# Kernel tuning notes

Measured on AMD Instinct MI355X. Metric: run time of the kernel, lower is better.

## Reference

```python
import jax, jax.numpy as jnp
import numpy as np

SIGMA_E, SIGMA_I, K_E, K_I = 0.6, 1.2, 0.8, 1.0
PM_STEPS, DT, BETA = 4, 0.15, 1.0
EPS = 1e-4


def setup_inputs() -> dict:
    key = jax.random.key(0)
    ks = jax.random.split(key, 12)
    B, d_in, d_lat, ch, d_out, n_c = 4096, 784, 8, 32, 10, 16
    inp = {
        "x": jax.random.normal(ks[0], (B, d_in), dtype=jnp.float32),
        "W1": jax.random.normal(ks[1], (d_in, 128), dtype=jnp.float32) * 0.03,
        "b1": jnp.zeros((128,), jnp.float32),
        "W2": jax.random.normal(ks[2], (128, d_lat), dtype=jnp.float32) * 0.08,
        "b2": jnp.zeros((d_lat,), jnp.float32),
        "centers": jax.random.normal(ks[3], (n_c, d_lat), dtype=jnp.float32) * 0.7,
        "mus": jnp.ones((n_c,), jnp.float32) * 0.5,
        "Wp": jax.random.normal(ks[4], (d_lat, ch), dtype=jnp.float32) * 0.3,
        "bp": jnp.zeros((ch,), jnp.float32),
        "Wr": jax.random.normal(ks[5], (ch, d_out), dtype=jnp.float32) * 0.15,
        "br": jnp.zeros((d_out,), jnp.float32),
        "T": 5,
    }
    return inp


def grad_ln_n(z, centers, mus):
    # z: [B,d], centers: [C,d], mus: [C]
    rvec = z[:, None, :] - centers[None, :, :]          # [B,C,d]
    r = jnp.sqrt(jnp.sum(rvec * rvec, axis=-1) + EPS)   # [B,C]
    n = 1.0 + jnp.sum(mus[None, :] / r, axis=1)          # [B]
    g = -jnp.sum((mus[None, :] / (r ** 3))[:, :, None] * rvec, axis=1)  # [B,d]
    return g / n[:, None]


def pm_field(z, centers, mus):
    for _ in range(PM_STEPS):
        z = jnp.clip(z + DT * BETA * grad_ln_n(z, centers, mus), -3.0, 3.0)
    return z


def lateral_kernel(z):
    # squared pairwise distances via the norm trick (avoids [B,B,d])
    sq = jnp.sum(z * z, axis=1)
    dist2 = jnp.maximum(sq[:, None] + sq[None, :] - 2.0 * (z @ z.T), 0.0)
    K = K_E * jnp.exp(-dist2 / (2.0 * SIGMA_E ** 2)) - K_I * jnp.exp(-dist2 / (2.0 * SIGMA_I ** 2))
    return jax.lax.stop_gradient(K)  # torch.no_grad in original


def reference(x, W1, b1, W2, b2, centers, mus, Wp, bp, Wr, br, T):
    B = x.shape[0]
    z = jnp.tanh(x.reshape(B, -1) @ W1 + b1) @ W2 + b2   # encoder
    h = jnp.zeros((B, Wr.shape[0]), x.dtype)
    for _ in range(T):
        z = pm_field(z, centers, mus)
        h = 0.9 * h + 0.1 * jnp.tanh(z @ Wp + bp)
        h = h + 0.05 * (lateral_kernel(z) @ h)
        y = h @ Wr + br
    return y
```

## Files before the change

### kernel.cpp

```cpp
#include <hip/hip_runtime.h>
#include <math.h>

#define NB    4096
#define DIN   784
#define DH    128
#define DL    8
#define NC    16
#define NCH   32
#define DO    10
#define TSTEPS 5

#define KH_ROWS   128
#define KH_JSLICE 64
#define KH_P      (NB / KH_JSLICE)
#define ENC_G     7

typedef float v2f __attribute__((ext_vector_type(2)));


__global__ __launch_bounds__(256) void enc1_kernel(const float* __restrict__ x,
    const float* __restrict__ W1, double* __restrict__ P)
{
    __shared__ float xsT[56][36];
    __shared__ float wss[56][128];
    const int tid = threadIdx.x;
    const int m0 = blockIdx.x * 32;
    const int kbeg = blockIdx.y * 112;
    const int cg = tid & 31, rg = tid >> 5;
    const int c0 = cg << 2, r0 = rg << 2;
    double acc[4][4] = {};
    for (int it = 0; it < 2; ++it) {
        const int k0 = kbeg + it * 56;
        __syncthreads();
        for (int l = tid; l < 448; l += 256) {
            int row = l / 14, f = l % 14;
            float4 v = *(const float4*)(x + (m0 + row) * DIN + k0 + f * 4);
            int kk = f * 4;
            xsT[kk][row] = v.x; xsT[kk + 1][row] = v.y;
            xsT[kk + 2][row] = v.z; xsT[kk + 3][row] = v.w;
        }
        for (int l = tid; l < 56 * 32; l += 256) {
            int kk = l >> 5, c = (l & 31) << 2;
            *(float4*)&wss[kk][c] = *(const float4*)(W1 + (k0 + kk) * DH + c);
        }
        __syncthreads();
#pragma unroll 8
        for (int kk = 0; kk < 56; ++kk) {
            const float4 xv = *(const float4*)&xsT[kk][r0];
            const float4 wv = *(const float4*)&wss[kk][c0];
            const double xr[4] = {(double)xv.x, (double)xv.y, (double)xv.z, (double)xv.w};
            const double wr[4] = {(double)wv.x, (double)wv.y, (double)wv.z, (double)wv.w};
#pragma unroll
            for (int i = 0; i < 4; ++i)
#pragma unroll
                for (int j = 0; j < 4; ++j)
                    acc[i][j] += xr[i] * wr[j];
        }
    }
    double* Pr = P + (size_t)blockIdx.y * (NB * DH);
#pragma unroll
    for (int i = 0; i < 4; ++i) {
        double* dst = Pr + (m0 + r0 + i) * DH + c0;
        *(double2*)dst       = make_double2(acc[i][0], acc[i][1]);
        *(double2*)(dst + 2) = make_double2(acc[i][2], acc[i][3]);
    }
}

__global__ __launch_bounds__(256) void enc2_kernel(const double* __restrict__ P,
    const float* __restrict__ b1, const float* __restrict__ W2,
    const float* __restrict__ b2, double* __restrict__ zbuf)
{
    __shared__ double As[16][132];
    __shared__ double W2d[DH * DL];
    const int tid = threadIdx.x;
    const int m0 = blockIdx.x * 16;
    for (int l = tid; l < DH * DL; l += 256) W2d[l] = (double)W2[l];
    for (int l = tid; l < 16 * 128; l += 256) {
        int row = l >> 7, k = l & 127;
        double v = (double)b1[k];
#pragma unroll
        for (int s = 0; s < ENC_G; ++s)
            v += P[(size_t)s * NB * DH + (m0 + row) * DH + k];
        As[row][k] = tanh(v);
    }
    __syncthreads();
    const int row = tid >> 4, d = (tid >> 1) & 7, half = tid & 1;
    double a = 0.0;
#pragma unroll 8
    for (int i = 0; i < 64; ++i) {
        const int k = half + (i << 1);
        a += As[row][k] * W2d[k * 8 + d];
    }
    a += __shfl_xor(a, 1);
    if (half == 0) zbuf[(m0 + row) * DL + d] = a + (double)b2[d];
}

__global__ __launch_bounds__(256) void enc_fused_kernel(const float* __restrict__ x,
    const float* __restrict__ W1, const float* __restrict__ b1,
    const float* __restrict__ W2, const float* __restrict__ b2,
    double* __restrict__ zbuf)
{
    __shared__ float  xsT[56][9];
    __shared__ float  wss[56][128];
    __shared__ double Asd[8][131];
    __shared__ double W2d[DH * DL];
    const int tid = threadIdx.x;
    const int m0 = blockIdx.x * 8;
    const int cg = tid & 31, rg = tid >> 5;
    const int c0 = cg << 2;
    for (int l = tid; l < DH * DL; l += 256) W2d[l] = (double)W2[l];
    double acc[4] = {};
    for (int it = 0; it < 14; ++it) {
        const int k0 = it * 56;
        __syncthreads();
        if (tid < 112) {
            int row = tid / 14, f = tid % 14;
            float4 v = *(const float4*)(x + (m0 + row) * DIN + k0 + f * 4);
            int kk = f * 4;
            xsT[kk][row] = v.x; xsT[kk + 1][row] = v.y;
            xsT[kk + 2][row] = v.z; xsT[kk + 3][row] = v.w;
        }
        for (int l = tid; l < 56 * 32; l += 256) {
            int kk = l >> 5, c = (l & 31) << 2;
            *(float4*)&wss[kk][c] = *(const float4*)(W1 + (k0 + kk) * DH + c);
        }
        __syncthreads();
#pragma unroll 8
        for (int kk = 0; kk < 56; ++kk) {
            const double xv = (double)xsT[kk][rg];
            const float4 wv = *(const float4*)&wss[kk][c0];
            acc[0] += xv * (double)wv.x;
            acc[1] += xv * (double)wv.y;
            acc[2] += xv * (double)wv.z;
            acc[3] += xv * (double)wv.w;
        }
    }
    __syncthreads();
#pragma unroll
    for (int j = 0; j < 4; ++j)
        Asd[rg][c0 + j] = tanh(acc[j] + (double)b1[c0 + j]);
    __syncthreads();
    {
        const int row = tid >> 5, d = (tid >> 2) & 7, kq = tid & 3;
        double a = 0.0;
#pragma unroll 8
        for (int i = 0; i < 32; ++i) {
            const int k = kq + (i << 2);
            a += Asd[row][k] * W2d[k * 8 + d];
        }
        a += __shfl_xor(a, 1);
        a += __shfl_xor(a, 2);
        if (kq == 0) zbuf[(m0 + row) * DL + d] = a + (double)b2[d];
    }
}

__global__ __launch_bounds__(64) void pmh_kernel(double* __restrict__ zbuf,
    const float* __restrict__ centers, const float* __restrict__ mus,
    const float* __restrict__ Wp, const float* __restrict__ bp,
    double* __restrict__ hB, float* __restrict__ zf, float* __restrict__ sqf,
    float* __restrict__ hAf, const float* __restrict__ part, int first)
{
    const int tid = threadIdx.x;
    const int lane = tid & 15;
    const int s = tid >> 4;
    const int i = blockIdx.x * 4 + s;
    double cz[8];
#pragma unroll
    for (int d = 0; d < 8; ++d) cz[d] = (double)centers[lane * DL + d];
    const double mu = (double)mus[lane];
    double z[8];
#pragma unroll
    for (int p = 0; p < 4; ++p) {
        double2 v = *(const double2*)(zbuf + i * DL + p * 2);
        z[p * 2] = v.x; z[p * 2 + 1] = v.y;
    }
#pragma unroll
    for (int st = 0; st < 4; ++st) {
        double rv[8];
        double ss = 1e-4;
#pragma unroll
        for (int d = 0; d < 8; ++d) { rv[d] = z[d] - cz[d]; ss += rv[d] * rv[d]; }
        double rinv = rsqrt(ss);
        double mr = mu * rinv;
        double n = mr;
        double mr3 = mr * (rinv * rinv);
        double g[8];
#pragma unroll
        for (int d = 0; d < 8; ++d) g[d] = -mr3 * rv[d];
#pragma unroll
        for (int m = 1; m < 16; m <<= 1) {
            n += __shfl_xor(n, m);
#pragma unroll
            for (int d = 0; d < 8; ++d) g[d] += __shfl_xor(g[d], m);
        }
        double sc = 0.15 / (1.0 + n);
#pragma unroll
        for (int d = 0; d < 8; ++d) z[d] = fmin(3.0, fmax(-3.0, z[d] + sc * g[d]));
    }
    if (lane == 0) {
        double sq = 0.0;
#pragma unroll
        for (int d = 0; d < 8; ++d) sq += z[d] * z[d];
        sqf[i] = (float)sq;
#pragma unroll
        for (int p = 0; p < 4; ++p)
            *(double2*)(zbuf + i * DL + p * 2) = make_double2(z[p * 2], z[p * 2 + 1]);
        float4 a = make_float4((float)z[0], (float)z[1], (float)z[2], (float)z[3]);
        float4 b = make_float4((float)z[4], (float)z[5], (float)z[6], (float)z[7]);
        *(float4*)(zf + i * DL)     = a;
        *(float4*)(zf + i * DL + 4) = b;
    }
#pragma unroll
    for (int cc = 0; cc < 2; ++cc) {
        const int c = lane + cc * 16;
        double a = (double)bp[c];
#pragma unroll
        for (int d = 0; d < 8; ++d) a += z[d] * (double)Wp[d * NCH + c];
        double ph = (double)tanhf((float)a);
        double prev = 0.0;
        if (!first) {
            prev = hB[i * NCH + c];
            if (part) {
                double sp = 0.0;
#pragma unroll 8
                for (int p = 0; p < KH_P; ++p)
                    sp += (double)part[(size_t)p * (NB * NCH) + i * NCH + c];
                prev += 0.05 * sp;
            }
        }
        double hv = 0.9 * prev + 0.1 * ph;
        hAf[i * NCH + c] = (float)hv;
        hB[i * NCH + c] = hv;
    }
}

#define SM_Z   0
#define SM_SQ  512
#define SM_H   576
#define SM_ALL 4224
__global__ __launch_bounds__(256) void kh_kernel(const float* __restrict__ zf,
    const float* __restrict__ sqf, const float* __restrict__ hAf,
    double* __restrict__ hB, float* __restrict__ part)
{
    __shared__ float smem[SM_ALL];
    const int tid = threadIdx.x;
    const int wave = tid >> 6, lane = tid & 63;
    const int row0 = blockIdx.x * KH_ROWS + lane;
    const int j0 = blockIdx.y * KH_JSLICE;
    float zr0[8], zr1[8];
    {
        float4 a = *(const float4*)(zf + row0 * 8);
        float4 b = *(const float4*)(zf + row0 * 8 + 4);
        zr0[0] = a.x; zr0[1] = a.y; zr0[2] = a.z; zr0[3] = a.w;
        zr0[4] = b.x; zr0[5] = b.y; zr0[6] = b.z; zr0[7] = b.w;
        float4 c = *(const float4*)(zf + (row0 + 64) * 8);
        float4 d = *(const float4*)(zf + (row0 + 64) * 8 + 4);
        zr1[0] = c.x; zr1[1] = c.y; zr1[2] = c.z; zr1[3] = c.w;
        zr1[4] = d.x; zr1[5] = d.y; zr1[6] = d.z; zr1[7] = d.w;
    }
    const float sq0 = sqf[row0], sq1 = sqf[row0 + 64];
    const float invI = 1.0f / 2.88f;
    if (tid < 128) {
        int jj = tid >> 1, p = (tid & 1) << 2;
        *(float4*)&smem[SM_Z + jj * 8 + p] = *(const float4*)(zf + (j0 + jj) * 8 + p);
    }
    if (tid < KH_JSLICE) smem[SM_SQ + tid] = sqf[j0 + tid];
    for (int l = tid; l < KH_JSLICE * 8; l += 256) {
        int jh = l >> 3, p = (l & 7) << 2;
        *(float4*)&smem[SM_H + jh * 32 + p] = *(const float4*)(hAf + (j0 + jh) * NCH + p);
    }
    __syncthreads();
    v2f a0[16], a1[16];
#pragma unroll
    for (int k = 0; k < 16; ++k) { a0[k] = (v2f)(0.f); a1[k] = (v2f)(0.f); }
    const int jjbeg = wave * 16;
#pragma unroll 2
    for (int q = 0; q < 16; ++q) {
        const int jj = jjbeg + q;
        const float4 a = *(const float4*)&smem[SM_Z + jj * 8];
        const float4 b = *(const float4*)&smem[SM_Z + jj * 8 + 4];
        const float sqj = smem[SM_SQ + jj];
        float dot0 = zr0[0] * a.x + zr0[1] * a.y + zr0[2] * a.z + zr0[3] * a.w
                   + zr0[4] * b.x + zr0[5] * b.y + zr0[6] * b.z + zr0[7] * b.w;
        float dot1 = zr1[0] * a.x + zr1[1] * a.y + zr1[2] * a.z + zr1[3] * a.w
                   + zr1[4] * b.x + zr1[5] * b.y + zr1[6] * b.z + zr1[7] * b.w;
        float d20 = fmaxf(sq0 + sqj - 2.0f * dot0, 0.0f);
        float d21 = fmaxf(sq1 + sqj - 2.0f * dot1, 0.0f);
        float e0 = __expf(-d20 * invI), e1 = __expf(-d21 * invI);
        float t0 = e0 * e0, t1 = e1 * e1;
        float K0 = 0.8f * (t0 * t0) - e0;
        float K1 = 0.8f * (t1 * t1) - e1;
        const v2f K0v = {K0, K0}, K1v = {K1, K1};
        const v2f* hrow = (const v2f*)&smem[SM_H + jj * 32];
#pragma unroll
        for (int k = 0; k < 16; k += 2) {
            const v2f h0 = hrow[k], h1 = hrow[k + 1];
            a0[k]     += K0v * h0; a0[k + 1] += K0v * h1;
            a1[k]     += K1v * h0; a1[k + 1] += K1v * h1;
        }
    }
    float* acc0 = (float*)a0;
    float* acc1 = (float*)a1;
    __syncthreads();
    if (wave == 1) {
#pragma unroll
        for (int c = 0; c < 32; ++c) { smem[lane * 33 + c] = acc0[c]; smem[(lane + 64) * 33 + c] = acc1[c]; }
    }
    __syncthreads();
    if (wave == 0) {
#pragma unroll
        for (int c = 0; c < 32; ++c) { acc0[c] += smem[lane * 33 + c]; acc1[c] += smem[(lane + 64) * 33 + c]; }
    }
    __syncthreads();
    if (wave == 3) {
#pragma unroll
        for (int c = 0; c < 32; ++c) { smem[lane * 33 + c] = acc0[c]; smem[(lane + 64) * 33 + c] = acc1[c]; }
    }
    __syncthreads();
    if (wave == 2) {
#pragma unroll
        for (int c = 0; c < 32; ++c) { acc0[c] += smem[lane * 33 + c]; acc1[c] += smem[(lane + 64) * 33 + c]; }
    }
    __syncthreads();
    if (wave == 2) {
#pragma unroll
        for (int c = 0; c < 32; ++c) { smem[lane * 33 + c] = acc0[c]; smem[(lane + 64) * 33 + c] = acc1[c]; }
    }
    __syncthreads();
    if (wave == 0) {
#pragma unroll
        for (int c = 0; c < 32; ++c) { acc0[c] += smem[lane * 33 + c]; acc1[c] += smem[(lane + 64) * 33 + c]; }
        if (part) {
            float* p0 = part + (size_t)blockIdx.y * (NB * NCH) + row0 * NCH;
            float* p1 = p0 + 64 * NCH;
#pragma unroll
            for (int c = 0; c < 32; c += 4) {
                *(float4*)(p0 + c) = make_float4(acc0[c], acc0[c + 1], acc0[c + 2], acc0[c + 3]);
                *(float4*)(p1 + c) = make_float4(acc1[c], acc1[c + 1], acc1[c + 2], acc1[c + 3]);
            }
        } else {
#pragma unroll
            for (int c = 0; c < 32; ++c) {
                atomicAdd(&hB[row0 * NCH + c], 0.05 * (double)acc0[c]);
                atomicAdd(&hB[(row0 + 64) * NCH + c], 0.05 * (double)acc1[c]);
            }
        }
    }
}

__global__ __launch_bounds__(256) void y_kernel(const double* __restrict__ h,
    const float* __restrict__ part, const float* __restrict__ Wr,
    const float* __restrict__ br, float* __restrict__ y)
{
    __shared__ double hsy[16][33];
    __shared__ double wrs[NCH * DO];
    __shared__ double brs[DO];
    const int tid = threadIdx.x;
    const int rb = blockIdx.x * 16;
    for (int l = tid; l < 16 * 32; l += 256) {
        int row = l >> 5, k = l & 31;
        const int gi = (rb + row) * NCH + k;
        double v = h[gi];
        if (part) {
            double sp = 0.0;
#pragma unroll 8
            for (int p = 0; p < KH_P; ++p) sp += (double)part[(size_t)p * (NB * NCH) + gi];
            v += 0.05 * sp;
        }
        hsy[row][k] = v;
    }
    for (int l = tid; l < NCH * DO; l += 256) wrs[l] = (double)Wr[l];
    if (tid < DO) brs[tid] = (double)br[tid];
    __syncthreads();
    const int row = tid >> 4, col = tid & 15;
    if (col < DO) {
        double a = brs[col];
#pragma unroll
        for (int k = 0; k < NCH; ++k) a += hsy[row][k] * wrs[k * DO + col];
        y[(rb + row) * DO + col] = (float)a;
    }
}

extern "C" void kernel_launch(void* const* d_in, const int* in_sizes, int n_in,
                              void* d_out, int out_size, void* d_ws, size_t ws_size,
                              hipStream_t stream)
{
    const float* x   = (const float*)d_in[0];
    const float* W1  = (const float*)d_in[1];
    const float* b1  = (const float*)d_in[2];
    const float* W2  = (const float*)d_in[3];
    const float* b2  = (const float*)d_in[4];
    const float* cen = (const float*)d_in[5];
    const float* mus = (const float*)d_in[6];
    const float* Wp  = (const float*)d_in[7];
    const float* bp  = (const float*)d_in[8];
    const float* Wr  = (const float*)d_in[9];
    const float* br  = (const float*)d_in[10];

    float* y = (float*)d_out;
    double* zbuf = (double*)d_ws;
    double* hB   = zbuf + NB * DL;
    float*  zf   = (float*)(hB + NB * NCH);
    float*  sqf  = zf + NB * DL;
    float*  hAf  = sqf + NB;
    float*  part = hAf + NB * NCH;
    double* Penc = (double*)(part + (size_t)KH_P * NB * NCH);

    const size_t need_part = (size_t)(NB * DL + NB * NCH) * 8
                           + (size_t)(NB * DL + NB + NB * NCH + (size_t)KH_P * NB * NCH) * 4;
    const size_t need_full = need_part + (size_t)ENC_G * NB * DH * 8;
    float* pp = (ws_size >= need_part) ? part : (float*)nullptr;

    if (ws_size >= need_full) {
        enc1_kernel<<<dim3(NB / 32, ENC_G), 256, 0, stream>>>(x, W1, Penc);
        enc2_kernel<<<NB / 16, 256, 0, stream>>>(Penc, b1, W2, b2, zbuf);
    } else {
        enc_fused_kernel<<<NB / 8, 256, 0, stream>>>(x, W1, b1, W2, b2, zbuf);
    }
    for (int t = 0; t < TSTEPS; ++t) {
        pmh_kernel<<<NB / 4, 64, 0, stream>>>(zbuf, cen, mus, Wp, bp, hB,
                                              zf, sqf, hAf, pp, t == 0 ? 1 : 0);
        kh_kernel<<<dim3(NB / KH_ROWS, KH_P), 256, 0, stream>>>(zf, sqf, hAf, hB, pp);
    }
    y_kernel<<<NB / 16, 256, 0, stream>>>(hB, pp, Wr, br, y);
}
```

Baseline: 367.1 us.

## Enlarge lateral-kernel tile to four rows per thread and double j-slice

The K·h kernel now has each thread hold four rows of z instead of two, and each block covers 256 rows and a 128-column j slice. Each loaded z/h row in shared memory is therefore reused across more accumulators. This halves the number of partial-sum slices that the downstream kernels must reduce and cuts the block count. In exchange, register pressure roughly doubles (128 float accumulators per thread) and there are fewer blocks to fill the GPU.

```diff
diff --git a/kernel.cpp b/kernel.cpp
--- a/kernel.cpp
+++ b/kernel.cpp
@@ -10,8 +10,8 @@
 #define DO    10
 #define TSTEPS 5
 
-#define KH_ROWS   128
-#define KH_JSLICE 64
+#define KH_ROWS   256
+#define KH_JSLICE 128
 #define KH_P      (NB / KH_JSLICE)
 #define ENC_G     7
 
@@ -222,7 +222,7 @@
             prev = hB[i * NCH + c];
             if (part) {
                 double sp = 0.0;
-#pragma unroll 8
+#pragma unroll
                 for (int p = 0; p < KH_P; ++p)
                     sp += (double)part[(size_t)p * (NB * NCH) + i * NCH + c];
                 prev += 0.05 * sp;
@@ -235,10 +235,10 @@
 }
 
 #define SM_Z   0
-#define SM_SQ  512
-#define SM_H   576
-#define SM_ALL 4224
-__global__ __launch_bounds__(256) void kh_kernel(const float* __restrict__ zf,
+#define SM_SQ  1024
+#define SM_H   1152
+#define SM_ALL 8448
+__global__ __launch_bounds__(256, 2) void kh_kernel(const float* __restrict__ zf,
     const float* __restrict__ sqf, const float* __restrict__ hAf,
     double* __restrict__ hB, float* __restrict__ part)
 {
@@ -247,20 +247,19 @@
     const int wave = tid >> 6, lane = tid & 63;
     const int row0 = blockIdx.x * KH_ROWS + lane;
     const int j0 = blockIdx.y * KH_JSLICE;
-    float zr0[8], zr1[8];
+    float zr[4][8];
+    float sqr[4];
+#pragma unroll
+    for (int i = 0; i < 4; ++i) {
+        const int r = row0 + 64 * i;
+        float4 a = *(const float4*)(zf + r * 8);
+        float4 b = *(const float4*)(zf + r * 8 + 4);
+        zr[i][0] = a.x; zr[i][1] = a.y; zr[i][2] = a.z; zr[i][3] = a.w;
+        zr[i][4] = b.x; zr[i][5] = b.y; zr[i][6] = b.z; zr[i][7] = b.w;
+        sqr[i] = sqf[r];
+    }
+    const float invI = 1.0f / 2.88f;
     {
-        float4 a = *(const float4*)(zf + row0 * 8);
-        float4 b = *(const float4*)(zf + row0 * 8 + 4);
-        zr0[0] = a.x; zr0[1] = a.y; zr0[2] = a.z; zr0[3] = a.w;
-        zr0[4] = b.x; zr0[5] = b.y; zr0[6] = b.z; zr0[7] = b.w;
-        float4 c = *(const float4*)(zf + (row0 + 64) * 8);
-        float4 d = *(const float4*)(zf + (row0 + 64) * 8 + 4);
-        zr1[0] = c.x; zr1[1] = c.y; zr1[2] = c.z; zr1[3] = c.w;
-        zr1[4] = d.x; zr1[5] = d.y; zr1[6] = d.z; zr1[7] = d.w;
-    }
-    const float sq0 = sqf[row0], sq1 = sqf[row0 + 64];
-    const float invI = 1.0f / 2.88f;
-    if (tid < 128) {
         int jj = tid >> 1, p = (tid & 1) << 2;
         *(float4*)&smem[SM_Z + jj * 8 + p] = *(const float4*)(zf + (j0 + jj) * 8 + p);
     }
@@ -270,79 +269,108 @@
         *(float4*)&smem[SM_H + jh * 32 + p] = *(const float4*)(hAf + (j0 + jh) * NCH + p);
     }
     __syncthreads();
-    v2f a0[16], a1[16];
-#pragma unroll
-    for (int k = 0; k < 16; ++k) { a0[k] = (v2f)(0.f); a1[k] = (v2f)(0.f); }
-    const int jjbeg = wave * 16;
+    v2f acc[4][16];
+#pragma unroll
+    for (int i = 0; i < 4; ++i)
+#pragma unroll
+        for (int k = 0; k < 16; ++k) acc[i][k] = (v2f)(0.f);
+    const int jjbeg = wave * 32;
 #pragma unroll 2
-    for (int q = 0; q < 16; ++q) {
+    for (int q = 0; q < 32; ++q) {
         const int jj = jjbeg + q;
         const float4 a = *(const float4*)&smem[SM_Z + jj * 8];
         const float4 b = *(const float4*)&smem[SM_Z + jj * 8 + 4];
         const float sqj = smem[SM_SQ + jj];
-        float dot0 = zr0[0] * a.x + zr0[1] * a.y + zr0[2] * a.z + zr0[3] * a.w
-                   + zr0[4] * b.x + zr0[5] * b.y + zr0[6] * b.z + zr0[7] * b.w;
-        float dot1 = zr1[0] * a.x + zr1[1] * a.y + zr1[2] * a.z + zr1[3] * a.w
-                   + zr1[4] * b.x + zr1[5] * b.y + zr1[6] * b.z + zr1[7] * b.w;
-        float d20 = fmaxf(sq0 + sqj - 2.0f * dot0, 0.0f);
-        float d21 = fmaxf(sq1 + sqj - 2.0f * dot1, 0.0f);
-        float e0 = __expf(-d20 * invI), e1 = __expf(-d21 * invI);
-        float t0 = e0 * e0, t1 = e1 * e1;
-        float K0 = 0.8f * (t0 * t0) - e0;
-        float K1 = 0.8f * (t1 * t1) - e1;
-        const v2f K0v = {K0, K0}, K1v = {K1, K1};
+        float K[4];
+#pragma unroll
+        for (int i = 0; i < 4; ++i) {
+            float dot = zr[i][0] * a.x + zr[i][1] * a.y + zr[i][2] * a.z + zr[i][3] * a.w
+                      + zr[i][4] * b.x + zr[i][5] * b.y + zr[i][6] * b.z + zr[i][7] * b.w;
+            float d2 = fmaxf(sqr[i] + sqj - 2.0f * dot, 0.0f);
+            float e = __expf(-d2 * invI);
+            float t = e * e;
+            K[i] = 0.8f * (t * t) - e;
+        }
         const v2f* hrow = (const v2f*)&smem[SM_H + jj * 32];
 #pragma unroll
         for (int k = 0; k < 16; k += 2) {
             const v2f h0 = hrow[k], h1 = hrow[k + 1];
-            a0[k]     += K0v * h0; a0[k + 1] += K0v * h1;
-            a1[k]     += K1v * h0; a1[k + 1] += K1v * h1;
-        }
-    }
-    float* acc0 = (float*)a0;
-    float* acc1 = (float*)a1;
+#pragma unroll
+            for (int i = 0; i < 4; ++i) {
+                const v2f Kv = {K[i], K[i]};
+                acc[i][k]     += Kv * h0;
+                acc[i][k + 1] += Kv * h1;
+            }
+        }
+    }
     __syncthreads();
     if (wave == 1) {
 #pragma unroll
-        for (int c = 0; c < 32; ++c) { smem[lane * 33 + c] = acc0[c]; smem[(lane + 64) * 33 + c] = acc1[c]; }
+        for (int i = 0; i < 4; ++i) {
+            float* a0 = (float*)acc[i];
+#pragma unroll
+            for (int c = 0; c < 32; ++c) smem[(lane + 64 * i) * 33 + c] = a0[c];
+        }
     }
     __syncthreads();
     if (wave == 0) {
 #pragma unroll
-        for (int c = 0; c < 32; ++c) { acc0[c] += smem[lane * 33 + c]; acc1[c] += smem[(lane + 64) * 33 + c]; }
+        for (int i = 0; i < 4; ++i) {
+            float* a0 = (float*)acc[i];
+#pragma unroll
+            for (int c = 0; c < 32; ++c) a0[c] += smem[(lane + 64 * i) * 33 + c];
+        }
     }
     __syncthreads();
     if (wave == 3) {
 #pragma unroll
-        for (int c = 0; c < 32; ++c) { smem[lane * 33 + c] = acc0[c]; smem[(lane + 64) * 33 + c] = acc1[c]; }
+        for (int i = 0; i < 4; ++i) {
+            float* a0 = (float*)acc[i];
+#pragma unroll
+            for (int c = 0; c < 32; ++c) smem[(lane + 64 * i) * 33 + c] = a0[c];
+        }
     }
     __syncthreads();
     if (wave == 2) {
 #pragma unroll
-        for (int c = 0; c < 32; ++c) { acc0[c] += smem[lane * 33 + c]; acc1[c] += smem[(lane + 64) * 33 + c]; }
+        for (int i = 0; i < 4; ++i) {
+            float* a0 = (float*)acc[i];
+#pragma unroll
+            for (int c = 0; c < 32; ++c) a0[c] += smem[(lane + 64 * i) * 33 + c];
+        }
     }
     __syncthreads();
     if (wave == 2) {
 #pragma unroll
-        for (int c = 0; c < 32; ++c) { smem[lane * 33 + c] = acc0[c]; smem[(lane + 64) * 33 + c] = acc1[c]; }
+        for (int i = 0; i < 4; ++i) {
+            float* a0 = (float*)acc[i];
+#pragma unroll
+            for (int c = 0; c < 32; ++c) smem[(lane + 64 * i) * 33 + c] = a0[c];
+        }
     }
     __syncthreads();
     if (wave == 0) {
-#pragma unroll
-        for (int c = 0; c < 32; ++c) { acc0[c] += smem[lane * 33 + c]; acc1[c] += smem[(lane + 64) * 33 + c]; }
         if (part) {
-            float* p0 = part + (size_t)blockIdx.y * (NB * NCH) + row0 * NCH;
-            float* p1 = p0 + 64 * NCH;
-#pragma unroll
-            for (int c = 0; c < 32; c += 4) {
-                *(float4*)(p0 + c) = make_float4(acc0[c], acc0[c + 1], acc0[c + 2], acc0[c + 3]);
-                *(float4*)(p1 + c) = make_float4(acc1[c], acc1[c + 1], acc1[c + 2], acc1[c + 3]);
+            float* pr = part + (size_t)blockIdx.y * (NB * NCH);
+#pragma unroll
+            for (int i = 0; i < 4; ++i) {
+                float* a0 = (float*)acc[i];
+#pragma unroll
+                for (int c = 0; c < 32; ++c) a0[c] += smem[(lane + 64 * i) * 33 + c];
+                float* p0 = pr + (row0 + 64 * i) * NCH;
+#pragma unroll
+                for (int c = 0; c < 32; c += 4)
+                    *(float4*)(p0 + c) = make_float4(a0[c], a0[c + 1], a0[c + 2], a0[c + 3]);
             }
         } else {
 #pragma unroll
-            for (int c = 0; c < 32; ++c) {
-                atomicAdd(&hB[row0 * NCH + c], 0.05 * (double)acc0[c]);
-                atomicAdd(&hB[(row0 + 64) * NCH + c], 0.05 * (double)acc1[c]);
+            for (int i = 0; i < 4; ++i) {
+                float* a0 = (float*)acc[i];
+#pragma unroll
+                for (int c = 0; c < 32; ++c) {
+                    a0[c] += smem[(lane + 64 * i) * 33 + c];
+                    atomicAdd(&hB[(row0 + 64 * i) * NCH + c], 0.05 * (double)a0[c]);
+                }
             }
         }
     }
@@ -363,7 +391,7 @@
         double v = h[gi];
         if (part) {
             double sp = 0.0;
-#pragma unroll 8
+#pragma unroll
             for (int p = 0; p < KH_P; ++p) sp += (double)part[(size_t)p * (NB * NCH) + gi];
             v += 0.05 * sp;
         }
```

Result: faster. 335.6 us (-8.6%).
